# Performance work log

Measured on AMD Instinct MI355X. Metric: run time of the kernel, lower is better.

Reference implementation:

```python
import jax, jax.numpy as jnp
import numpy as np

B, L, C_IN, C_OUT = 16, 1024, 21, 21
D_MODEL, EXPAND, D_STATE, D_CONV = 512, 2, 16, 4
D_INNER = D_MODEL * EXPAND
DT_RANK = (D_MODEL + 15) // 16  # math.ceil(d_model/16) = 32
PRED_LEN = 96
N_MARK = 4  # freq='h' -> 4 time features


def setup_inputs() -> dict:
    key = jax.random.key(0)
    ks = jax.random.split(key, 16)
    s = 0.02
    return {
        "x_enc": jax.random.normal(ks[0], (B, L, C_IN), jnp.float32),
        "x_mark_enc": jax.random.uniform(ks[1], (B, L, N_MARK), jnp.float32) - 0.5,
        # DataEmbedding params
        "conv_tok_w": jax.random.normal(ks[2], (3, C_IN, D_MODEL), jnp.float32) * s,  # kernel=3 circular conv
        "time_w": jax.random.normal(ks[3], (N_MARK, D_MODEL), jnp.float32) * s,
        # Mamba params
        "W_in": jax.random.normal(ks[4], (D_MODEL, 2 * D_INNER), jnp.float32) * s,
        "conv_w": jax.random.normal(ks[5], (D_INNER, D_CONV), jnp.float32) * s,  # depthwise causal conv
        "conv_b": jnp.zeros((D_INNER,), jnp.float32),
        "W_xproj": jax.random.normal(ks[6], (D_INNER, DT_RANK + 2 * D_STATE), jnp.float32) * s,
        "W_dt": jax.random.normal(ks[7], (DT_RANK, D_INNER), jnp.float32) * s,
        "b_dt": jax.random.normal(ks[8], (D_INNER,), jnp.float32) * s,
        "A_log": jnp.log(jnp.tile(jnp.arange(1, D_STATE + 1, dtype=jnp.float32)[None, :], (D_INNER, 1))),
        "D": jnp.ones((D_INNER,), jnp.float32),
        "W_out": jax.random.normal(ks[9], (D_INNER, D_MODEL), jnp.float32) * s,
        # output head
        "W_head": jax.random.normal(ks[10], (D_MODEL, C_OUT), jnp.float32) * s,
    }


def _pos_embedding(l, d):
    pos = jnp.arange(l, dtype=jnp.float32)[:, None]
    div = jnp.exp(jnp.arange(0, d, 2, dtype=jnp.float32) * (-jnp.log(10000.0) / d))
    pe = jnp.zeros((l, d), jnp.float32)
    pe = pe.at[:, 0::2].set(jnp.sin(pos * div))
    pe = pe.at[:, 1::2].set(jnp.cos(pos * div))
    return pe


def _forward(x_enc, x_mark_enc, conv_tok_w, time_w, W_in, conv_w, conv_b,
             W_xproj, W_dt, b_dt, A_log, D, W_out, W_head):
    # RevIN (stats detached)
    mean = jax.lax.stop_gradient(jnp.mean(x_enc, axis=1, keepdims=True))
    xc = x_enc - mean
    std = jax.lax.stop_gradient(jnp.sqrt(jnp.var(xc, axis=1, keepdims=True) + 1e-5))
    xn = xc / std

    # TokenEmbedding: Conv1d k=3, circular padding, no bias
    xp = jnp.pad(xn, ((0, 0), (1, 1), (0, 0)), mode="wrap")
    tok = sum(jnp.einsum("blc,cd->bld", xp[:, k:k + L, :], conv_tok_w[k]) for k in range(3))
    emb = tok + x_mark_enc @ time_w + _pos_embedding(L, D_MODEL)[None]

    # Mamba block
    xz = emb @ W_in                      # [B, L, 2*d_inner]
    u, z = jnp.split(xz, 2, axis=-1)
    # depthwise causal conv (left pad d_conv-1, truncate to L) + SiLU
    upad = jnp.pad(u, ((0, 0), (D_CONV - 1, 0), (0, 0)))
    u = sum(upad[:, k:k + L, :] * conv_w[:, k] for k in range(D_CONV)) + conv_b
    u = u * jax.nn.sigmoid(u)

    x_dbl = u @ W_xproj                  # [B, L, dt_rank + 2*d_state]
    dtr, Bm, Cm = jnp.split(x_dbl, [DT_RANK, DT_RANK + D_STATE], axis=-1)
    dt = jax.nn.softplus(dtr @ W_dt + b_dt)   # [B, L, d_inner]
    A = -jnp.exp(A_log)                       # [d_inner, d_state]

    def step(h, inp):
        u_t, dt_t, B_t, C_t = inp             # [B,d_inner],[B,d_inner],[B,S],[B,S]
        dA = jnp.exp(dt_t[..., None] * A)     # [B, d_inner, d_state]
        h = h * dA + (dt_t * u_t)[..., None] * B_t[:, None, :]
        y = jnp.einsum("bds,bs->bd", h, C_t)
        return h, y

    h0 = jnp.zeros((B, D_INNER, D_STATE), u.dtype)
    xs = (u.transpose(1, 0, 2), dt.transpose(1, 0, 2),
          Bm.transpose(1, 0, 2), Cm.transpose(1, 0, 2))
    _, ys = jax.lax.scan(step, h0, xs)        # [L, B, d_inner]
    y = ys.transpose(1, 0, 2) + u * D
    y = y * (z * jax.nn.sigmoid(z))           # gated by SiLU(z)
    mout = y @ W_out                          # [B, L, d_model]

    out = (mout @ W_head) * std + mean        # de-normalize
    return out[:, -PRED_LEN:, :]


def reference(x_enc, x_mark_enc, conv_tok_w, time_w, W_in, conv_w, conv_b,
              W_xproj, W_dt, b_dt, A_log, D, W_out, W_head):
    return _forward(x_enc, x_mark_enc, conv_tok_w, time_w, W_in, conv_w, conv_b,
                    W_xproj, W_dt, b_dt, A_log, D, W_out, W_head)
```

## Files before the change

kernel.cpp:

```cpp
#include <hip/hip_runtime.h>
#include <hip/hip_bf16.h>
#include <cstddef>
#include <cstdint>
#include <cmath>

#define BB 16
#define LL 1024
#define CIN 21
#define COUT 21
#define DMODEL 512
#define DINNER 1024
#define DSTATE 16
#define PRED 96
#define NTOK (BB * LL)
#define CHL 64
#define NCH 14
#define LHEAD 896
#define NTC 8
#define NHI 6
#define LOUT 928
#define KEMB 96

typedef __attribute__((ext_vector_type(8))) short short8;
typedef __attribute__((ext_vector_type(4))) float floatx4;

struct P3 {
  const short* a1; const short* b1; void* c1;
  const short* a2; const short* b2; void* c2;
  const short* a3; const short* b3; void* c3;
};

__device__ __forceinline__ float bf2f(unsigned short u) {
  return __uint_as_float(((unsigned int)u) << 16);
}
__device__ __forceinline__ unsigned short f2bf_bits(float f) {
  __hip_bfloat16 h = __float2bfloat16(f);
  return *(unsigned short*)&h;
}
__device__ __forceinline__ float fast_softplus(float x) {
  if (x > 20.f) return x;
  const float t = __builtin_amdgcn_exp2f(x * 1.44269504089f);
  return 0.69314718056f * __builtin_amdgcn_logf(1.f + t);
}

#define S_WIN (2048 * 512)
#define S_WX (64 * 1024)
#define S_WDT (1024 * 32)
#define S_WO (512 * 1024)
#define S_WTE (128 * 512)
#define S_PE (LL * DMODEL)
#define S_WHT (128 * 512)
#define PREP_TOT \
  (S_WIN + S_WX + S_WDT + S_WO + S_WTE + S_PE + S_WHT)
#define PREP_BLOCKS (PREP_TOT / 256)

__global__ __launch_bounds__(256) void prep_all(
    const float* __restrict__ W_in, const float* __restrict__ W_xproj,
    const float* __restrict__ W_dt, const float* __restrict__ W_out,
    const float* __restrict__ Wtok, const float* __restrict__ Wtime,
    const float* __restrict__ W_head, const float* __restrict__ x,
    __hip_bfloat16* __restrict__ WinT, __hip_bfloat16* __restrict__ WxT,
    __hip_bfloat16* __restrict__ WdtT, __hip_bfloat16* __restrict__ WoT,
    __hip_bfloat16* __restrict__ WtE2, __hip_bfloat16* __restrict__ peb,
    __hip_bfloat16* __restrict__ WhT, float* __restrict__ meanv,
    float* __restrict__ stdv, float* __restrict__ rstdv) {
  __shared__ float ss[256], sqq[256];
  if (blockIdx.x >= PREP_BLOCKS) {
    const int idx = blockIdx.x - PREP_BLOCKS;
    const int b = idx / CIN, c = idx % CIN;
    const int tid = threadIdx.x;
    float s = 0.f, sq = 0.f;
    for (int l = tid; l < LL; l += 256) {
      float v = x[((size_t)b * LL + l) * CIN + c];
      s += v;
      sq += v * v;
    }
    ss[tid] = s;
    sqq[tid] = sq;
    __syncthreads();
    for (int off = 128; off > 0; off >>= 1) {
      if (tid < off) {
        ss[tid] += ss[tid + off];
        sqq[tid] += sqq[tid + off];
      }
      __syncthreads();
    }
    if (tid == 0) {
      float m = ss[0] * (1.f / LL);
      float var = sqq[0] * (1.f / LL) - m * m;
      var = fmaxf(var, 0.f);
      float sd = sqrtf(var + 1e-5f);
      meanv[idx] = m;
      stdv[idx] = sd;
      rstdv[idx] = 1.f / sd;
    }
    return;
  }
  int i = blockIdx.x * 256 + threadIdx.x;
  if (i < S_WIN) {
    const int n = i >> 9, k = i & 511;
    WinT[i] = __float2bfloat16(W_in[(size_t)k * 2048 + n]);
    return;
  }
  i -= S_WIN;
  if (i < S_WX) {
    const int n = i >> 10, k = i & 1023;
    WxT[i] = __float2bfloat16(W_xproj[(size_t)k * 64 + n]);
    return;
  }
  i -= S_WX;
  if (i < S_WDT) {
    const int d = i >> 5, r = i & 31;
    WdtT[i] = __float2bfloat16(W_dt[(size_t)r * 1024 + d]);
    return;
  }
  i -= S_WDT;
  if (i < S_WO) {
    const int n = i >> 10, k = i & 1023;
    WoT[i] = __float2bfloat16(W_out[(size_t)k * 512 + n]);
    return;
  }
  i -= S_WO;
  if (i < S_WTE) {
    const int j = i >> 9, d = i & 511;
    float val = 0.f;
    if (j < 63)
      val = Wtok[(size_t)j * DMODEL + d];
    else if (j < 67)
      val = Wtime[(size_t)(j - 63) * DMODEL + d];
    WtE2[i] = __float2bfloat16(val);
    return;
  }
  i -= S_WTE;
  if (i < S_PE) {
    const int d = i & (DMODEL - 1);
    const int l = i >> 9;
    const float freq = __expf((float)(d & ~1) * (-9.210340371976184f / 512.f));
    const float ang = (float)l * freq;
    peb[i] = __float2bfloat16((d & 1) ? __cosf(ang) : __sinf(ang));
    return;
  }
  i -= S_PE;
  {
    const int c = i >> 9, m = i & 511;
    WhT[i] = __float2bfloat16((c < COUT) ? W_head[(size_t)m * COUT + c] : 0.f);
  }
}

__global__ __launch_bounds__(256) void build_xfeat(
    const float* __restrict__ x, const float* __restrict__ xmark,
    const float* __restrict__ meanv, const float* __restrict__ rstdv,
    __hip_bfloat16* __restrict__ Xf) {
  const int i = blockIdx.x * 256 + threadIdx.x;
  const int row = i / KEMB, j = i - row * KEMB;
  const int b = row >> 10, l = row & (LL - 1);
  float val = 0.f;
  if (j < 63) {
    const int k = (j >= 42) ? 2 : ((j >= 21) ? 1 : 0);
    const int c = j - k * 21;
    int ls = l + k - 1;
    if (ls < 0) ls += LL;
    if (ls >= LL) ls -= LL;
    val = (x[((size_t)b * LL + ls) * CIN + c] - meanv[b * CIN + c]) *
          rstdv[b * CIN + c];
  } else if (j < 67) {
    val = xmark[((size_t)row) * 4 + (j - 63)];
  }
  Xf[i] = __float2bfloat16(val);
}

enum { EPI_XD = 2, EPI_OUT = 6, EPI_P3 = 7, EPI_UCONVZ = 8 };

template <int BM, int BN, int BK, int EPI>
__global__ __launch_bounds__(256) void gemm_mfma(
    const short* __restrict__ A_, const short* __restrict__ BT_, int K,
    void* __restrict__ C0v, void* __restrict__ C1v, int ldc_, int bnoff,
    const float* __restrict__ Cw, const float* __restrict__ Cb, P3 p3) {
  constexpr int TI = BM / 32, TJ = BN / 32;
  constexpr int CPR = BK / 8;
  constexpr int NA = (BM * CPR) / 256;
  constexpr int NB = (BN * CPR) / 256;
  __shared__ short Asm[BM * BK];
  __shared__ short Bsm[BN * BK];
  __shared__ __align__(16) short Ut[(EPI == EPI_UCONVZ) ? 131 * 128 : 1];
  const int tid = threadIdx.x;
  const int wave = tid >> 6, lane = tid & 63;
  const int wm = wave & 1, wn = wave >> 1;
  const int m16 = lane & 15, quad = lane >> 4;
  const short* A = A_;
  const short* BT = BT_;
  void* C0 = C0v;
  int ldc = ldc_;
  int bm = blockIdx.x * BM;
  int bn = blockIdx.y * BN + bnoff;
  int Mg = 1 << 30, Ng = 1 << 30;
  bool isZ = false;
  if constexpr (EPI == EPI_P3) {
    const int x = blockIdx.x;
    if (x < 128) {
      A = p3.a1; BT = p3.b1; C0 = p3.c1; ldc = 2048;
      bm = (x & 7) * 128; bn = (x >> 3) * 128;
    } else if (x < 144) {
      A = p3.a2; BT = p3.b2; C0 = p3.c2; ldc = 96;
      bm = (x - 128) * 128; bn = 0; Ng = 96;
    } else {
      A = p3.a3; BT = p3.b3; C0 = p3.c3; ldc = 1024;
      bm = 0; bn = (x - 144) * 128; Mg = 32;
    }
  }
  if constexpr (EPI == EPI_UCONVZ) {
    if (blockIdx.x >= 128) {
      isZ = true;
      bm = (blockIdx.x - 128) * BM;
      bn = blockIdx.y * BN + DINNER;
    }
  }
  floatx4 acc[TI][TJ];
#pragma unroll
  for (int i = 0; i < TI; ++i)
#pragma unroll
    for (int j = 0; j < TJ; ++j) acc[i][j] = (floatx4){0.f, 0.f, 0.f, 0.f};
  const int cbase = wave * 64 + lane;
  const int kc = (cbase % CPR) * 8;
  const short* aptr[NA];
  const short* bptr[NB];
#pragma unroll
  for (int p = 0; p < NA; ++p) {
    int row = bm + p * (256 / CPR) + cbase / CPR;
    if constexpr (EPI == EPI_UCONVZ) {
      if (isZ) {
        const int bb = row / PRED;
        row = bb * LL + LOUT + (row - bb * PRED);
      }
    }
    aptr[p] = A + (size_t)row * K + kc;
  }
#pragma unroll
  for (int p = 0; p < NB; ++p)
    bptr[p] = BT + (size_t)(bn + p * (256 / CPR) + cbase / CPR) * K + kc;
  for (int k0 = 0; k0 < K; k0 += BK) {
#pragma unroll
    for (int p = 0; p < NA; ++p)
      __builtin_amdgcn_global_load_lds(
          (const __attribute__((address_space(1))) void*)(aptr[p] + k0),
          (__attribute__((address_space(3))) void*)(Asm + p * 2048 + wave * 512),
          16, 0, 0);
#pragma unroll
    for (int p = 0; p < NB; ++p)
      __builtin_amdgcn_global_load_lds(
          (const __attribute__((address_space(1))) void*)(bptr[p] + k0),
          (__attribute__((address_space(3))) void*)(Bsm + p * 2048 + wave * 512),
          16, 0, 0);
    __syncthreads();
#pragma unroll
    for (int ks = 0; ks < BK / 32; ++ks) {
      short8 af[TI], bf[TJ];
#pragma unroll
      for (int i = 0; i < TI; ++i)
        af[i] = *(const short8*)(Asm + (wm * (BM / 2) + i * 16 + m16) * BK +
                                 ks * 32 + quad * 8);
#pragma unroll
      for (int j = 0; j < TJ; ++j)
        bf[j] = *(const short8*)(Bsm + (wn * (BN / 2) + j * 16 + m16) * BK +
                                 ks * 32 + quad * 8);
#pragma unroll
      for (int i = 0; i < TI; ++i)
#pragma unroll
        for (int j = 0; j < TJ; ++j)
          acc[i][j] = __builtin_amdgcn_mfma_f32_16x16x32_bf16(af[i], bf[j],
                                                              acc[i][j], 0, 0,
                                                              0);
    }
    __syncthreads();
  }
  if constexpr (EPI == EPI_UCONVZ) {
    if (!isZ) {
      const int l0 = bm & (LL - 1);
      const int bb = bm >> 10;
      const unsigned short* peB = (const unsigned short*)C1v;
#pragma unroll
      for (int i = 0; i < TI; ++i) {
        const int lr0 = wm * (BM / 2) + i * 16 + quad * 4;
#pragma unroll
        for (int j = 0; j < TJ; ++j) {
          const int dc = wn * (BN / 2) + j * 16 + m16;
          const int gn = bn + dc;
#pragma unroll
          for (int r = 0; r < 4; ++r) {
            const int lr = lr0 + r;
            const float p = bf2f(peB[(size_t)(l0 + lr) * 2048 + gn]);
            Ut[(lr + 3) * 128 + dc] = (short)f2bf_bits(acc[i][j][r] + p);
          }
        }
      }
      for (int e = tid; e < 384; e += 256) {
        const int hr = e >> 7, dc = e & 127;
        float v = 0.f;
        if (l0 > 0) {
          const int gl = l0 - 3 + hr;
          const short* xr = A + (size_t)(bb * LL + gl) * K;
          const short* wr = BT + (size_t)(bn + dc) * K;
          float s = 0.f;
          for (int k = 0; k < KEMB; ++k)
            s = fmaf(bf2f((unsigned short)xr[k]), bf2f((unsigned short)wr[k]),
                     s);
          v = s + bf2f(peB[(size_t)gl * 2048 + bn + dc]);
        }
        Ut[hr * 128 + dc] = (short)f2bf_bits(v);
      }
      __syncthreads();
      const int d8 = tid & 15, lg = tid >> 4;
      const int dl0 = d8 * 8;
      float w[8][4], bias[8];
      const float4* cw4 = (const float4*)Cw;
#pragma unroll
      for (int j = 0; j < 8; ++j) {
        const float4 t = cw4[bn + dl0 + j];
        w[j][0] = t.x; w[j][1] = t.y; w[j][2] = t.z; w[j][3] = t.w;
        bias[j] = Cb[bn + dl0 + j];
      }
#pragma unroll
      for (int t = 0; t < 8; ++t) {
        const int ll = lg * 8 + t;
        float av[8];
#pragma unroll
        for (int j = 0; j < 8; ++j) av[j] = bias[j];
#pragma unroll
        for (int k = 0; k < 4; ++k) {
          const uint4 rv = *(const uint4*)(Ut + (ll + k) * 128 + dl0);
          const unsigned int uu[4] = {rv.x, rv.y, rv.z, rv.w};
#pragma unroll
          for (int j = 0; j < 8; ++j) {
            const unsigned short hv =
                (unsigned short)(uu[j >> 1] >> ((j & 1) * 16));
            av[j] = fmaf(bf2f(hv), w[j][k], av[j]);
          }
        }
        unsigned int outp[4];
#pragma unroll
        for (int jj = 0; jj < 4; ++jj) {
          float a0 = av[2 * jj], a1 = av[2 * jj + 1];
          a0 = a0 / (1.f + __expf(-a0));
          a1 = a1 / (1.f + __expf(-a1));
          outp[jj] = ((unsigned int)f2bf_bits(a1) << 16) | f2bf_bits(a0);
        }
        *(uint4*)((__hip_bfloat16*)C0 + (size_t)(bb * LL + l0 + ll) * DINNER +
                  bn + dl0) = make_uint4(outp[0], outp[1], outp[2], outp[3]);
      }
    } else {
      const unsigned short* peB = (const unsigned short*)C1v;
      float* zc = (float*)p3.c1;
#pragma unroll
      for (int i = 0; i < TI; ++i) {
        const int gm0 = bm + wm * (BM / 2) + i * 16 + quad * 4;
#pragma unroll
        for (int j = 0; j < TJ; ++j) {
          const int gn = bn + wn * (BN / 2) + j * 16 + m16;
#pragma unroll
          for (int r = 0; r < 4; ++r) {
            const int gm = gm0 + r;
            const float p =
                bf2f(peB[(size_t)(LOUT + (gm % PRED)) * 2048 + gn]);
            zc[(size_t)gm * DINNER + (gn - DINNER)] = acc[i][j][r] + p;
          }
        }
      }
    }
    return;
  } else {
#pragma unroll
    for (int i = 0; i < TI; ++i) {
      const int gm0 = bm + wm * (BM / 2) + i * 16 + quad * 4;
#pragma unroll
      for (int j = 0; j < TJ; ++j) {
        const int gn = bn + wn * (BN / 2) + j * 16 + m16;
#pragma unroll
        for (int r = 0; r < 4; ++r) {
          const int gm = gm0 + r;
          const float v = acc[i][j][r];
          if (EPI == EPI_P3) {
            if (gm < Mg && gn < Ng)
              ((__hip_bfloat16*)C0)[(size_t)gm * ldc + gn] =
                  __float2bfloat16(v);
          } else if (EPI == EPI_XD) {
            ((float*)C0)[(size_t)gm * ldc + gn] = v;
            if (gn < 32)
              ((__hip_bfloat16*)C1v)[(size_t)gm * 32 + gn] =
                  __float2bfloat16(v);
          } else if (EPI == EPI_OUT) {
            if (gn < COUT) {
              const float* st = (const float*)C1v;
              const int bq = gm / PRED;
              ((float*)C0)[(size_t)gm * COUT + gn] =
                  v * st[BB * CIN + bq * CIN + gn] + st[bq * CIN + gn];
            }
          } else {
            ((float*)C0)[(size_t)gm * ldc + gn] = v;
          }
        }
      }
    }
  }
}

template <int CHLT>
__device__ __forceinline__ void scan_body(
    const float* __restrict__ x_dbl, const short* __restrict__ dtrb,
    const unsigned short* __restrict__ ub, const short* __restrict__ WdtT,
    const float* __restrict__ b_dt, const float* __restrict__ A_log,
    float* __restrict__ Qo, float* __restrict__ SDo, int l0, int ch, int nch,
    int b, int dbase, unsigned short (*us)[128], unsigned short (*dts)[128]) {
  constexpr int LP = (CHLT > 32) ? 32 : CHLT;
  constexpr int NP = CHLT / LP;
  const int tid = threadIdx.x;
  const int wave = tid >> 6, lane = tid & 63;
  const int m16 = lane & 15, quad = lane >> 4;
  const int d = dbase + tid;
  const float A0 = -__expf(A_log[(size_t)d * DSTATE]);
  const float A0l2e = A0 * 1.44269504089f;
  short8 wf[4];
#pragma unroll
  for (int nt = 0; nt < 4; ++nt)
    wf[nt] = *(const short8*)(WdtT +
                              (size_t)(dbase + wave * 64 + nt * 16 + m16) * 32 +
                              quad * 8);
  float Q[16];
#pragma unroll
  for (int s = 0; s < 16; ++s) Q[s] = 0.f;
  float sumdt = 0.f;
  const float4* xb = (const float4*)(x_dbl + ((size_t)(b * LL + l0)) * 64 + 32);
  for (int hp = 0; hp < NP; ++hp) {
    const int lb = l0 + hp * LP;
    {
      const uint4* src =
          (const uint4*)(ub + ((size_t)(b * LL + lb)) * DINNER + dbase);
      uint4* dst = (uint4*)&us[0][0];
#pragma unroll
      for (int k = 0; k < LP / 8; ++k) {
        const int j = k * 128 + tid;
        dst[j] = src[(size_t)(j >> 4) * 128 + (j & 15)];
      }
    }
    {
      short8 af[LP / 16];
#pragma unroll
      for (int mt = 0; mt < LP / 16; ++mt)
        af[mt] = *(const short8*)(dtrb +
                                  (size_t)(b * LL + lb + mt * 16 + m16) * 32 +
                                  quad * 8);
#pragma unroll
      for (int nt = 0; nt < 4; ++nt) {
        const int col = wave * 64 + nt * 16 + m16;
        const float bb = b_dt[dbase + col];
#pragma unroll
        for (int mt = 0; mt < LP / 16; ++mt) {
          floatx4 a = (floatx4){0.f, 0.f, 0.f, 0.f};
          a = __builtin_amdgcn_mfma_f32_16x16x32_bf16(af[mt], wf[nt], a, 0, 0,
                                                      0);
#pragma unroll
          for (int r = 0; r < 4; ++r)
            dts[mt * 16 + quad * 4 + r][col] =
                f2bf_bits(fast_softplus(a[r] + bb));
        }
      }
    }
    __syncthreads();
#pragma unroll 8
    for (int ll = 0; ll < LP; ++ll) {
      const float dt = bf2f(dts[ll][tid]);
      const float uu = bf2f(us[ll][tid]);
      const float dtu = dt * uu;
      sumdt += dt;
      const int lx = hp * LP + ll;
      const float4 B0 = xb[lx * 16 + 0], B1 = xb[lx * 16 + 1];
      const float4 B2 = xb[lx * 16 + 2], B3 = xb[lx * 16 + 3];
      const float Bv[16] = {B0.x, B0.y, B0.z, B0.w, B1.x, B1.y, B1.z, B1.w,
                            B2.x, B2.y, B2.z, B2.w, B3.x, B3.y, B3.z, B3.w};
      float pwv[16];
      pwv[0] = __builtin_amdgcn_exp2f(dt * A0l2e);
      pwv[1] = pwv[0] * pwv[0];
      pwv[2] = pwv[1] * pwv[0];
      pwv[3] = pwv[1] * pwv[1];
      pwv[4] = pwv[3] * pwv[0];
      pwv[5] = pwv[3] * pwv[1];
      pwv[6] = pwv[3] * pwv[2];
      pwv[7] = pwv[3] * pwv[3];
      pwv[8] = pwv[7] * pwv[0];
      pwv[9] = pwv[7] * pwv[1];
      pwv[10] = pwv[7] * pwv[2];
      pwv[11] = pwv[7] * pwv[3];
      pwv[12] = pwv[7] * pwv[4];
      pwv[13] = pwv[7] * pwv[5];
      pwv[14] = pwv[7] * pwv[6];
      pwv[15] = pwv[7] * pwv[7];
#pragma unroll
      for (int s = 0; s < 16; ++s) Q[s] = fmaf(Q[s], pwv[s], dtu * Bv[s]);
    }
    __syncthreads();
  }
  float4* qdst = (float4*)(Qo + (((size_t)b * nch + ch) * DINNER + d) * DSTATE);
#pragma unroll
  for (int k = 0; k < 4; ++k)
    qdst[k] = make_float4(Q[4 * k], Q[4 * k + 1], Q[4 * k + 2], Q[4 * k + 3]);
  SDo[((size_t)b * nch + ch) * DINNER + d] = sumdt;
}

__global__ __launch_bounds__(128) void scan_chunks_all(
    const float* __restrict__ x_dbl, const short* __restrict__ dtrb,
    const unsigned short* __restrict__ ub, const short* __restrict__ WdtT,
    const float* __restrict__ b_dt, const float* __restrict__ A_log,
    float* __restrict__ Qh, float* __restrict__ SDh, float* __restrict__ Qt,
    float* __restrict__ SDt) {
  __shared__ unsigned short us[32][128];
  __shared__ unsigned short dts[32][128];
  const int dbase = blockIdx.x * 128;
  const int y = blockIdx.y, b = blockIdx.z;
  if (y < NCH) {
    scan_body<CHL>(x_dbl, dtrb, ub, WdtT, b_dt, A_log, Qh, SDh, y * CHL, y,
                   NCH, b, dbase, us, dts);
  } else {
    const int tc = y - NCH;
    scan_body<16>(x_dbl, dtrb, ub, WdtT, b_dt, A_log, Qt, SDt,
                  LHEAD + tc * 16, tc, NTC, b, dbase, us, dts);
  }
}

__global__ __launch_bounds__(256) void scan_combine(
    const float* __restrict__ Qh, const float* __restrict__ SDh,
    const float* __restrict__ Qt, const float* __restrict__ SDt,
    const float* __restrict__ A_log, float* __restrict__ hinit) {
  const int i = blockIdx.x * 256 + threadIdx.x;
  const int b = i >> 14, ds = i & 16383;
  const int d = ds >> 4, s = ds & 15;
  const float A0l2e_s =
      -__expf(A_log[(size_t)d * DSTATE]) * 1.44269504089f * (float)(s + 1);
  float h = 0.f;
  for (int c = 0; c < NCH; ++c) {
    const float q = Qh[(((size_t)b * NCH + c) << 14) + ds];
    const float sd = SDh[((size_t)b * NCH + c) * DINNER + d];
    h = fmaf(h, __builtin_amdgcn_exp2f(sd * A0l2e_s), q);
  }
#pragma unroll
  for (int tc = 0; tc < NTC; ++tc) {
    if (tc >= 2) hinit[(((size_t)b * NHI + (tc - 2)) << 14) + ds] = h;
    const float q = Qt[(((size_t)b * NTC + tc) << 14) + ds];
    const float sd = SDt[((size_t)b * NTC + tc) * DINNER + d];
    h = fmaf(h, __builtin_amdgcn_exp2f(sd * A0l2e_s), q);
  }
}

__global__ __launch_bounds__(64) void scan_y(
    const float* __restrict__ x_dbl, const unsigned short* __restrict__ ub,
    const float* __restrict__ z_last, const float* __restrict__ W_dt,
    const float* __restrict__ b_dt, const float* __restrict__ A_log,
    const float* __restrict__ Dp, const float* __restrict__ hinit,
    __hip_bfloat16* __restrict__ Ag) {
  const int b = blockIdx.z, tc = blockIdx.y;
  const int d = blockIdx.x * 64 + threadIdx.x;
  float wdt[32];
#pragma unroll
  for (int k = 0; k < 32; ++k) wdt[k] = W_dt[k * DINNER + d];
  const float bdt = b_dt[d];
  const float A0 = -__expf(A_log[(size_t)d * DSTATE]);
  const float A0l2e = A0 * 1.44269504089f;
  const float Dd = Dp[d];
  float h[16];
  {
    const float4* hp =
        (const float4*)(hinit + (((size_t)b * NHI + tc) << 14) + d * 16);
#pragma unroll
    for (int k = 0; k < 4; ++k) {
      const float4 v = hp[k];
      h[4 * k] = v.x;
      h[4 * k + 1] = v.y;
      h[4 * k + 2] = v.z;
      h[4 * k + 3] = v.w;
    }
  }
#pragma unroll 4
  for (int t = 0; t < 16; ++t) {
    const int l = LOUT + tc * 16 + t;
    const float4* xr = (const float4*)(x_dbl + ((size_t)(b * LL + l)) * 64);
    float a0 = bdt, a1 = 0.f, a2 = 0.f, a3 = 0.f;
#pragma unroll
    for (int k4 = 0; k4 < 8; k4 += 4) {
      const float4 x0 = xr[k4], x1 = xr[k4 + 1], x2 = xr[k4 + 2],
                   x3 = xr[k4 + 3];
      a0 = fmaf(x0.w, wdt[k4 * 4 + 3],
           fmaf(x0.z, wdt[k4 * 4 + 2],
           fmaf(x0.y, wdt[k4 * 4 + 1], fmaf(x0.x, wdt[k4 * 4], a0))));
      a1 = fmaf(x1.w, wdt[k4 * 4 + 7],
           fmaf(x1.z, wdt[k4 * 4 + 6],
           fmaf(x1.y, wdt[k4 * 4 + 5], fmaf(x1.x, wdt[k4 * 4 + 4], a1))));
      a2 = fmaf(x2.w, wdt[k4 * 4 + 11],
           fmaf(x2.z, wdt[k4 * 4 + 10],
           fmaf(x2.y, wdt[k4 * 4 + 9], fmaf(x2.x, wdt[k4 * 4 + 8], a2))));
      a3 = fmaf(x3.w, wdt[k4 * 4 + 15],
           fmaf(x3.z, wdt[k4 * 4 + 14],
           fmaf(x3.y, wdt[k4 * 4 + 13], fmaf(x3.x, wdt[k4 * 4 + 12], a3))));
    }
    const float dt = fast_softplus((a0 + a1) + (a2 + a3));
    const float uu = bf2f(ub[((size_t)(b * LL + l)) * DINNER + d]);
    const float dtu = dt * uu;
    const float w = __builtin_amdgcn_exp2f(dt * A0l2e);
    const float4 B0 = xr[8], B1 = xr[9], B2 = xr[10], B3 = xr[11];
    const float4 C0 = xr[12], C1 = xr[13], C2 = xr[14], C3 = xr[15];
    const float Bv[16] = {B0.x, B0.y, B0.z, B0.w, B1.x, B1.y, B1.z, B1.w,
                          B2.x, B2.y, B2.z, B2.w, B3.x, B3.y, B3.z, B3.w};
    const float Cv[16] = {C0.x, C0.y, C0.z, C0.w, C1.x, C1.y, C1.z, C1.w,
                          C2.x, C2.y, C2.z, C2.w, C3.x, C3.y, C3.z, C3.w};
    float wk = w, y = 0.f;
#pragma unroll
    for (int s = 0; s < 16; ++s) {
      if (s > 0) wk *= w;
      h[s] = fmaf(h[s], wk, dtu * Bv[s]);
      y = fmaf(h[s], Cv[s], y);
    }
    const int gr = b * PRED + tc * 16 + t;
    const float zz = z_last[(size_t)gr * DINNER + d];
    const float gate = zz / (1.f + __expf(-zz));
    Ag[(size_t)gr * DINNER + d] = __float2bfloat16(fmaf(uu, Dd, y) * gate);
  }
}

extern "C" void kernel_launch(void* const* d_in, const int* in_sizes, int n_in,
                              void* d_out, int out_size, void* d_ws,
                              size_t ws_size, hipStream_t stream) {
  (void)in_sizes; (void)n_in; (void)out_size; (void)ws_size;
  const float* x_enc = (const float*)d_in[0];
  const float* x_mark = (const float*)d_in[1];
  const float* Wtok = (const float*)d_in[2];
  const float* Wtime = (const float*)d_in[3];
  const float* W_in = (const float*)d_in[4];
  const float* conv_w = (const float*)d_in[5];
  const float* conv_b = (const float*)d_in[6];
  const float* W_xproj = (const float*)d_in[7];
  const float* W_dt = (const float*)d_in[8];
  const float* b_dt = (const float*)d_in[9];
  const float* A_log = (const float*)d_in[10];
  const float* Dp = (const float*)d_in[11];
  const float* W_out = (const float*)d_in[12];
  const float* W_head = (const float*)d_in[13];
  float* out = (float*)d_out;

  char* ws = (char*)d_ws;
  __hip_bfloat16* ub = (__hip_bfloat16*)(ws + ((size_t)32 << 20));
  __hip_bfloat16* pe_inb = (__hip_bfloat16*)(ws + ((size_t)64 << 20));
  __hip_bfloat16* W_combT = (__hip_bfloat16*)(ws + ((size_t)70 << 20));
  __hip_bfloat16* W_ohT = (__hip_bfloat16*)(ws + ((size_t)72 << 20));
  __hip_bfloat16* WhT = (__hip_bfloat16*)(ws + ((size_t)73 << 20));
  __hip_bfloat16* WinT = (__hip_bfloat16*)(ws + ((size_t)80 << 20));
  __hip_bfloat16* WxT = (__hip_bfloat16*)(ws + ((size_t)82 << 20));
  __hip_bfloat16* WdtT = (__hip_bfloat16*)(ws + ((size_t)83 << 20));
  __hip_bfloat16* WoT = (__hip_bfloat16*)(ws + ((size_t)84 << 20));
  float* x_dbl = (float*)(ws + ((size_t)85 << 20));
  __hip_bfloat16* dtrb = (__hip_bfloat16*)(ws + ((size_t)89 << 20));
  float* z_last = (float*)(ws + ((size_t)90 << 20));
  float* Qh = (float*)(ws + ((size_t)96 << 20));
  float* Qt = (float*)(ws + ((size_t)112 << 20));
  float* SDh = (float*)(ws + ((size_t)121 << 20));
  float* SDt = (float*)(ws + ((size_t)122 << 20));
  float* hinit = (float*)(ws + ((size_t)124 << 20));
  __hip_bfloat16* Ag = (__hip_bfloat16*)(ws + ((size_t)143 << 20));
  __hip_bfloat16* Xf = (__hip_bfloat16*)(ws + ((size_t)149 << 20));
  __hip_bfloat16* WtE2 = (__hip_bfloat16*)(ws + ((size_t)152 << 20));
  __hip_bfloat16* peb = (__hip_bfloat16*)(ws + ((size_t)153 << 20));
  float* stats = (float*)(ws + ((size_t)156 << 20));
  float* meanv = stats;
  float* stdv = stats + BB * CIN;
  float* rstdv = stats + 2 * BB * CIN;

  const P3 p3empty = {};

  prep_all<<<dim3(PREP_BLOCKS + BB * CIN), 256, 0, stream>>>(
      W_in, W_xproj, W_dt, W_out, Wtok, Wtime, W_head, x_enc, WinT, WxT, WdtT,
      WoT, WtE2, peb, WhT, meanv, stdv, rstdv);
  build_xfeat<<<dim3(NTOK * KEMB / 256), 256, 0, stream>>>(x_enc, x_mark,
                                                           meanv, rstdv, Xf);
  {
    P3 p3;
    p3.a1 = (const short*)peb;  p3.b1 = (const short*)WinT; p3.c1 = pe_inb;
    p3.a2 = (const short*)WinT; p3.b2 = (const short*)WtE2; p3.c2 = W_combT;
    p3.a3 = (const short*)WhT;  p3.b3 = (const short*)WoT;  p3.c3 = W_ohT;
    gemm_mfma<128, 128, 64, EPI_P3><<<dim3(152), 256, 0, stream>>>(
        nullptr, nullptr, 512, nullptr, nullptr, 0, 0, nullptr, nullptr, p3);
  }
  {
    P3 p3 = {};
    p3.c1 = z_last;
    gemm_mfma<128, 128, 32, EPI_UCONVZ><<<dim3(140, 8), 256, 0, stream>>>(
        (const short*)Xf, (const short*)W_combT, KEMB, ub, pe_inb, DINNER, 0,
        conv_w, conv_b, p3);
  }
  gemm_mfma<64, 64, 64, EPI_XD><<<dim3(256, 1), 256, 0, stream>>>(
      (const short*)ub, (const short*)WxT, 1024, x_dbl, dtrb, 64, 0, nullptr,
      nullptr, p3empty);
  scan_chunks_all<<<dim3(DINNER / 128, NCH + NTC, BB), 128, 0, stream>>>(
      x_dbl, (const short*)dtrb, (const unsigned short*)ub, (const short*)WdtT,
      b_dt, A_log, Qh, SDh, Qt, SDt);
  scan_combine<<<dim3(BB * DINNER * DSTATE / 256), 256, 0, stream>>>(
      Qh, SDh, Qt, SDt, A_log, hinit);
  scan_y<<<dim3(DINNER / 64, NHI, BB), 64, 0, stream>>>(
      x_dbl, (const unsigned short*)ub, z_last, W_dt, b_dt, A_log, Dp, hinit,
      Ag);
  gemm_mfma<64, 32, 64, EPI_OUT><<<dim3(24, 1), 256, 0, stream>>>(
      (const short*)Ag, (const short*)W_ohT, 1024, out, stats, COUT, 0,
      nullptr, nullptr, p3empty);
}
```

Measured before the change: 233.5 us.

## Precompute positional-embedding conv contribution in P3 and alias LDS buffers

Uses linearity of the depthwise causal conv to precompute, in the weight-prep GEMM kernel, the conv of the positional-embedding projection plus the conv bias into a table PCb. The main UCONVZ epilogue then loads that table as the accumulator's initial value instead of gathering per-element pe_inb values before the conv. Shared memory for the A/B tiles and the Ut staging buffer is merged into one aliased pool to cut LDS footprint, and the halo dot products are vectorised to short8 loads. This adds conv work to the small prep kernel and relies on correct reuse of the LDS pool after the main loop's final sync.

```diff
diff --git a/kernel.cpp b/kernel.cpp
--- a/kernel.cpp
+++ b/kernel.cpp
@@ -180,9 +180,13 @@
   constexpr int CPR = BK / 8;
   constexpr int NA = (BM * CPR) / 256;
   constexpr int NB = (BN * CPR) / 256;
-  __shared__ short Asm[BM * BK];
-  __shared__ short Bsm[BN * BK];
-  __shared__ __align__(16) short Ut[(EPI == EPI_UCONVZ) ? 131 * 128 : 1];
+  constexpr int LDSM = BM * BK + BN * BK;
+  constexpr bool NEEDUT = (EPI == EPI_UCONVZ) || (EPI == EPI_P3);
+  constexpr int PSZ = NEEDUT ? (LDSM > 131 * 128 ? LDSM : 131 * 128) : LDSM;
+  __shared__ __align__(16) short pool[PSZ];
+  short* Asm = pool;
+  short* Bsm = pool + BM * BK;
+  short* Ut = pool;
   const int tid = threadIdx.x;
   const int wave = tid >> 6, lane = tid & 63;
   const int wm = wave & 1, wn = wave >> 1;
@@ -273,24 +277,106 @@
     }
     __syncthreads();
   }
-  if constexpr (EPI == EPI_UCONVZ) {
+  if constexpr (EPI == EPI_P3) {
+    if (blockIdx.x < 64) {
+#pragma unroll
+      for (int i = 0; i < TI; ++i) {
+        const int lr0 = wm * (BM / 2) + i * 16 + quad * 4;
+#pragma unroll
+        for (int j = 0; j < TJ; ++j) {
+          const int dc = wn * (BN / 2) + j * 16 + m16;
+#pragma unroll
+          for (int r = 0; r < 4; ++r)
+            Ut[(lr0 + r + 3) * 128 + dc] = (short)f2bf_bits(acc[i][j][r]);
+        }
+      }
+      for (int e = tid; e < 384; e += 256) {
+        const int hr = e >> 7, dc = e & 127;
+        float v = 0.f;
+        if (bm > 0) {
+          const int gl = bm - 3 + hr;
+          const short8* xr8 = (const short8*)(A + (size_t)gl * K);
+          const short8* wr8 = (const short8*)(BT + (size_t)(bn + dc) * K);
+          float s = 0.f;
+#pragma unroll 8
+          for (int c = 0; c < 64; ++c) {
+            const short8 a = xr8[c], w = wr8[c];
+#pragma unroll
+            for (int q = 0; q < 8; ++q)
+              s = fmaf(bf2f((unsigned short)a[q]), bf2f((unsigned short)w[q]),
+                       s);
+          }
+          v = s;
+        }
+        Ut[hr * 128 + dc] = (short)f2bf_bits(v);
+      }
+      __syncthreads();
+      const int d8 = tid & 15, lg = tid >> 4;
+      const int dl0 = d8 * 8;
+      float w[8][4], bias[8];
+      const float4* cw4 = (const float4*)Cw;
+#pragma unroll
+      for (int j = 0; j < 8; ++j) {
+        const float4 t = cw4[bn + dl0 + j];
+        w[j][0] = t.x; w[j][1] = t.y; w[j][2] = t.z; w[j][3] = t.w;
+        bias[j] = Cb[bn + dl0 + j];
+      }
+#pragma unroll
+      for (int t = 0; t < 8; ++t) {
+        const int ll = lg * 8 + t;
+        float av[8];
+#pragma unroll
+        for (int j = 0; j < 8; ++j) av[j] = bias[j];
+#pragma unroll
+        for (int k = 0; k < 4; ++k) {
+          const uint4 rv = *(const uint4*)(Ut + (ll + k) * 128 + dl0);
+          const unsigned int uu[4] = {rv.x, rv.y, rv.z, rv.w};
+#pragma unroll
+          for (int j = 0; j < 8; ++j) {
+            const unsigned short hv =
+                (unsigned short)(uu[j >> 1] >> ((j & 1) * 16));
+            av[j] = fmaf(bf2f(hv), w[j][k], av[j]);
+          }
+        }
+        unsigned int outp[4];
+#pragma unroll
+        for (int jj = 0; jj < 4; ++jj)
+          outp[jj] = ((unsigned int)f2bf_bits(av[2 * jj + 1]) << 16) |
+                     f2bf_bits(av[2 * jj]);
+        *(uint4*)((__hip_bfloat16*)C0v + (size_t)(bm + ll) * 1024 + bn + dl0) =
+            make_uint4(outp[0], outp[1], outp[2], outp[3]);
+      }
+      return;
+    }
+#pragma unroll
+    for (int i = 0; i < TI; ++i) {
+      const int gm0 = bm + wm * (BM / 2) + i * 16 + quad * 4;
+#pragma unroll
+      for (int j = 0; j < TJ; ++j) {
+        const int gn = bn + wn * (BN / 2) + j * 16 + m16;
+#pragma unroll
+        for (int r = 0; r < 4; ++r) {
+          const int gm = gm0 + r;
+          if (gm < Mg && gn < Ng)
+            ((__hip_bfloat16*)C0)[(size_t)gm * ldc + gn] =
+                __float2bfloat16(acc[i][j][r]);
+        }
+      }
+    }
+    return;
+  } else if constexpr (EPI == EPI_UCONVZ) {
     if (!isZ) {
       const int l0 = bm & (LL - 1);
       const int bb = bm >> 10;
-      const unsigned short* peB = (const unsigned short*)C1v;
 #pragma unroll
       for (int i = 0; i < TI; ++i) {
         const int lr0 = wm * (BM / 2) + i * 16 + quad * 4;
 #pragma unroll
         for (int j = 0; j < TJ; ++j) {
           const int dc = wn * (BN / 2) + j * 16 + m16;
-          const int gn = bn + dc;
-#pragma unroll
-          for (int r = 0; r < 4; ++r) {
-            const int lr = lr0 + r;
-            const float p = bf2f(peB[(size_t)(l0 + lr) * 2048 + gn]);
-            Ut[(lr + 3) * 128 + dc] = (short)f2bf_bits(acc[i][j][r] + p);
-          }
+#pragma unroll
+          for (int r = 0; r < 4; ++r)
+            Ut[(lr0 + r + 3) * 128 + dc] = (short)f2bf_bits(acc[i][j][r]);
         }
       }
       for (int e = tid; e < 384; e += 256) {
@@ -298,33 +384,44 @@
         float v = 0.f;
         if (l0 > 0) {
           const int gl = l0 - 3 + hr;
-          const short* xr = A + (size_t)(bb * LL + gl) * K;
-          const short* wr = BT + (size_t)(bn + dc) * K;
+          const short8* xr8 = (const short8*)(A + (size_t)(bb * LL + gl) * K);
+          const short8* wr8 = (const short8*)(BT + (size_t)(bn + dc) * K);
           float s = 0.f;
-          for (int k = 0; k < KEMB; ++k)
-            s = fmaf(bf2f((unsigned short)xr[k]), bf2f((unsigned short)wr[k]),
-                     s);
-          v = s + bf2f(peB[(size_t)gl * 2048 + bn + dc]);
+#pragma unroll 4
+          for (int c = 0; c < 12; ++c) {
+            const short8 a = xr8[c], w = wr8[c];
+#pragma unroll
+            for (int q = 0; q < 8; ++q)
+              s = fmaf(bf2f((unsigned short)a[q]), bf2f((unsigned short)w[q]),
+                       s);
+          }
+          v = s;
         }
         Ut[hr * 128 + dc] = (short)f2bf_bits(v);
       }
       __syncthreads();
+      const unsigned short* PCb = (const unsigned short*)p3.c2;
       const int d8 = tid & 15, lg = tid >> 4;
       const int dl0 = d8 * 8;
-      float w[8][4], bias[8];
+      float w[8][4];
       const float4* cw4 = (const float4*)Cw;
 #pragma unroll
       for (int j = 0; j < 8; ++j) {
         const float4 t = cw4[bn + dl0 + j];
         w[j][0] = t.x; w[j][1] = t.y; w[j][2] = t.z; w[j][3] = t.w;
-        bias[j] = Cb[bn + dl0 + j];
       }
 #pragma unroll
       for (int t = 0; t < 8; ++t) {
         const int ll = lg * 8 + t;
         float av[8];
-#pragma unroll
-        for (int j = 0; j < 8; ++j) av[j] = bias[j];
+        {
+          const uint4 pv =
+              *(const uint4*)(PCb + (size_t)(l0 + ll) * 1024 + bn + dl0);
+          const unsigned int pu[4] = {pv.x, pv.y, pv.z, pv.w};
+#pragma unroll
+          for (int j = 0; j < 8; ++j)
+            av[j] = bf2f((unsigned short)(pu[j >> 1] >> ((j & 1) * 16)));
+        }
 #pragma unroll
         for (int k = 0; k < 4; ++k) {
           const uint4 rv = *(const uint4*)(Ut + (ll + k) * 128 + dl0);
@@ -378,11 +475,7 @@
         for (int r = 0; r < 4; ++r) {
           const int gm = gm0 + r;
           const float v = acc[i][j][r];
-          if (EPI == EPI_P3) {
-            if (gm < Mg && gn < Ng)
-              ((__hip_bfloat16*)C0)[(size_t)gm * ldc + gn] =
-                  __float2bfloat16(v);
-          } else if (EPI == EPI_XD) {
+          if (EPI == EPI_XD) {
             ((float*)C0)[(size_t)gm * ldc + gn] = v;
             if (gn < 32)
               ((__hip_bfloat16*)C1v)[(size_t)gm * 32 + gn] =
@@ -649,6 +742,7 @@
   __hip_bfloat16* W_combT = (__hip_bfloat16*)(ws + ((size_t)70 << 20));
   __hip_bfloat16* W_ohT = (__hip_bfloat16*)(ws + ((size_t)72 << 20));
   __hip_bfloat16* WhT = (__hip_bfloat16*)(ws + ((size_t)73 << 20));
+  __hip_bfloat16* PCb = (__hip_bfloat16*)(ws + ((size_t)76 << 20));
   __hip_bfloat16* WinT = (__hip_bfloat16*)(ws + ((size_t)80 << 20));
   __hip_bfloat16* WxT = (__hip_bfloat16*)(ws + ((size_t)82 << 20));
   __hip_bfloat16* WdtT = (__hip_bfloat16*)(ws + ((size_t)83 << 20));
@@ -683,11 +777,12 @@
     p3.a2 = (const short*)WinT; p3.b2 = (const short*)WtE2; p3.c2 = W_combT;
     p3.a3 = (const short*)WhT;  p3.b3 = (const short*)WoT;  p3.c3 = W_ohT;
     gemm_mfma<128, 128, 64, EPI_P3><<<dim3(152), 256, 0, stream>>>(
-        nullptr, nullptr, 512, nullptr, nullptr, 0, 0, nullptr, nullptr, p3);
+        nullptr, nullptr, 512, PCb, nullptr, 0, 0, conv_w, conv_b, p3);
   }
   {
     P3 p3 = {};
     p3.c1 = z_last;
+    p3.c2 = PCb;
     gemm_mfma<128, 128, 32, EPI_UCONVZ><<<dim3(140, 8), 256, 0, stream>>>(
         (const short*)Xf, (const short*)W_combT, KEMB, ub, pe_inb, DINNER, 0,
         conv_w, conv_b, p3);
```

New measurement: 254.5 us. 9.0% more time.
